# Kernel optimization log

Measured on AMD Instinct MI355X. Metric: run time of the kernel, lower is better.

The kernel has to match this reference:

```python
import jax, jax.numpy as jnp
import numpy as np

N, P, IN, HID, HEADS, OUT, E = 8192, 3, 256, 64, 8, 64, 262144
HD = HEADS * HID


def _gat(h, fc, al, ar, bias, src, dst):
    # DGL GATConv forward (no dropout), returns (elu(out) [N,H,D], attention [E,H])
    feat = (h @ fc).reshape(N, HEADS, HID)          # [N,H,D]
    el = (feat * al).sum(-1)                        # [N,H]
    er = (feat * ar).sum(-1)                        # [N,H]
    e = jax.nn.leaky_relu(el[src] + er[dst], negative_slope=0.2)  # [E,H]
    emax = jax.ops.segment_max(e, dst, num_segments=N)            # [N,H]
    ee = jnp.exp(e - emax[dst])
    denom = jax.ops.segment_sum(ee, dst, num_segments=N)          # [N,H]
    a = ee / denom[dst]                                           # edge softmax over dst
    rst = jax.ops.segment_sum(a[:, :, None] * feat[src], dst, num_segments=N)  # [N,H,D]
    out = jax.nn.elu(rst + bias)
    return out, a


def setup_inputs():
    key = jax.random.key(0)
    ks = jax.random.split(key, 12)
    s = 0.05
    return {
        "h": jax.random.normal(ks[0], (N, IN), jnp.float32),
        "edge_src": jax.random.randint(ks[1], (P, E), 0, N, jnp.int32),
        "edge_dst": jax.random.randint(ks[2], (P, E), 0, N, jnp.int32),
        "gat_fc": jax.random.normal(ks[3], (P, IN, HD), jnp.float32) * s,
        "attn_l": jax.random.normal(ks[4], (P, HEADS, HID), jnp.float32) * s,
        "attn_r": jax.random.normal(ks[5], (P, HEADS, HID), jnp.float32) * s,
        "gat_bias": jnp.zeros((P, HEADS, HID), jnp.float32),
        "sa_w1": jax.random.normal(ks[6], (HD, 128), jnp.float32) * s,
        "sa_b1": jnp.zeros((128,), jnp.float32),
        "sa_w2": jax.random.normal(ks[7], (128, 1), jnp.float32) * s,
        "pred_w": jax.random.normal(ks[8], (HD, OUT), jnp.float32) * s,
        "pred_b": jnp.zeros((OUT,), jnp.float32),
    }


def reference(h, edge_src, edge_dst, gat_fc, attn_l, attn_r, gat_bias,
              sa_w1, sa_b1, sa_w2, pred_w, pred_b):
    zp_list, alpha_list = [], []
    for p in range(P):
        z_p, a_p = _gat(h, gat_fc[p], attn_l[p], attn_r[p], gat_bias[p],
                        edge_src[p], edge_dst[p])
        zp_list.append(z_p.reshape(N, HD))          # flatten(start_dim=1)
        alpha_list.append(a_p.mean(axis=1))         # [E], mean over heads
    zp = jnp.stack(zp_list, axis=1)                 # [N,P,HD]

    # Semantic attention
    w = (zp @ sa_w1 + sa_b1) @ sa_w2                # [N,P,1]
    w = jax.nn.leaky_relu(w, negative_slope=0.01).mean(axis=0)  # [P,1]
    beta = jax.nn.softmax(w, axis=0)                # [P,1]

    # Dense adjacency accumulation of edge attention weights
    atten = jnp.zeros((N, N), jnp.float32)
    for p in range(P):
        vals = alpha_list[p] * beta[p, 0]
        atten = atten.at[edge_src[p], edge_dst[p]].add(vals)

    z = (beta[None, :, :] * zp).sum(axis=1)         # [N,HD]
    out = z @ pred_w + pred_b                       # [N,OUT]
    return out, atten
```

## Files before the change

kernel.cpp:

```cpp
#include <hip/hip_runtime.h>
#include <math.h>

#define NN    8192
#define PP    3
#define INF_  256
#define HID_  64
#define HEADS 8
#define OUTF  64
#define NE    262144
#define HD    512
#define DEGCAP 128
#define NB    4
#define DOFF  (NB * NN)
#define POFF  (NB * NN + 1)

typedef __attribute__((ext_vector_type(8))) short short8;
typedef __attribute__((ext_vector_type(4))) float f32x4;

__device__ __forceinline__ unsigned short f2bf(float f) {
    unsigned u = __float_as_uint(f);
    unsigned r = u + 0x7fffu + ((u >> 16) & 1u);
    return (unsigned short)(r >> 16);
}
__device__ __forceinline__ float bf2f_lo(unsigned v) { return __uint_as_float(v << 16); }
__device__ __forceinline__ float bf2f_hi(unsigned v) { return __uint_as_float(v & 0xffff0000u); }

__device__ __forceinline__ void beta_reg(const float* __restrict__ wsum,
                                         float& rb0, float& rb1, float& rb2) {
    int lane = threadIdx.x & 63;
    float s0 = wsum[lane], s1 = wsum[64 + lane], s2 = wsum[128 + lane];
#pragma unroll
    for (int off = 32; off > 0; off >>= 1) {
        s0 += __shfl_down(s0, off);
        s1 += __shfl_down(s1, off);
        s2 += __shfl_down(s2, off);
    }
    float t0 = __shfl(s0, 0), t1 = __shfl(s1, 0), t2 = __shfl(s2, 0);
    float w0 = t0 / (float)NN, w1 = t1 / (float)NN, w2 = t2 / (float)NN;
    float m  = fmaxf(w0, fmaxf(w1, w2));
    float e0 = expf(w0 - m), e1 = expf(w1 - m), e2 = expf(w2 - m);
    float ss = e0 + e1 + e2;
    rb0 = e0 / ss; rb1 = e1 / ss; rb2 = e2 / ss;
}

__global__ __launch_bounds__(256) void cast_count(
        const float* __restrict__ h, const float* __restrict__ fc,
        const int* __restrict__ esrc, const int* __restrict__ edst,
        unsigned short* __restrict__ hb, unsigned short* __restrict__ fcT,
        int* __restrict__ counts ,
        float* __restrict__ atten) {
    int b = blockIdx.x, t = threadIdx.x;
    if (b < 2048) {
        int i = b * 256 + t;
        float4 v = *(const float4*)(h + (size_t)i * 4);
        ushort4 o = { f2bf(v.x), f2bf(v.y), f2bf(v.z), f2bf(v.w) };
        *(ushort4*)(hb + (size_t)i * 4) = o;
    } else if (b < 2048 + 1536) {
        int i = (b - 2048) * 256 + t;
        if (i < PP * INF_ * HD) {
            int p = i / (INF_ * HD);
            int rem = i - p * INF_ * HD;
            int k = rem / HD;
            int n = rem - k * HD;
            fcT[(size_t)p * HD * INF_ + (size_t)n * INF_ + k] = f2bf(fc[i]);
        }
    } else if (b < 2048 + 1536 + 768) {
        int i = (b - 3584) * 256 + t;
        int4 s4 = ((const int4*)esrc)[i];
        int4 d4 = ((const int4*)edst)[i];
        int p = i >> 16;
        int base = p * DOFF;
        atomicAdd(&counts[base + (d4.x << 2) + (s4.x >> 11)], 1);
        atomicAdd(&counts[base + (d4.y << 2) + (s4.y >> 11)], 1);
        atomicAdd(&counts[base + (d4.z << 2) + (s4.z >> 11)], 1);
        atomicAdd(&counts[base + (d4.w << 2) + (s4.w >> 11)], 1);
    } else {
        f32x4* a4 = (f32x4*)atten;
        int idx0 = (b - 4352) * 256 + t;
        f32x4 zero = {0.f, 0.f, 0.f, 0.f};
#pragma unroll 4
        for (int it = 0; it < 64; ++it)
            __builtin_nontemporal_store(zero, &a4[(size_t)it * 262144 + idx0]);
    }
}

__global__ __launch_bounds__(1024) void scan_vw(
        const int* __restrict__ counts, int* __restrict__ offsets,
        int* __restrict__ cursor, const float* __restrict__ w1,
        const float* __restrict__ b1, const float* __restrict__ w2,
        float* __restrict__ v ) {
    int t = threadIdx.x;
    if (blockIdx.x == 3) {
        if (t < HD) {
            float s = 0.f;
            for (int k = 0; k < 128; ++k) s += w1[t * 128 + k] * w2[k];
            v[t] = s;
        } else if (t == HD) {
            float c = 0.f;
            for (int k = 0; k < 128; ++k) c += b1[k] * w2[k];
            v[HD] = c;
        }
        return;
    }
    __shared__ int sh[1024];
    int seg = blockIdx.x;
    const int* cnt = counts + seg * DOFF;
    int* offs = offsets + seg * POFF;
    int* cur  = cursor + seg * DOFF;
    int loc[32];
    int s = 0;
#pragma unroll
    for (int i = 0; i < 32; ++i) { loc[i] = cnt[t * 32 + i]; s += loc[i]; }
    sh[t] = s;
    __syncthreads();
    for (int off = 1; off < 1024; off <<= 1) {
        int vv = (t >= off) ? sh[t - off] : 0;
        __syncthreads();
        sh[t] += vv;
        __syncthreads();
    }
    int run = sh[t] - s;
#pragma unroll
    for (int i = 0; i < 32; ++i) {
        offs[t * 32 + i] = run;
        cur[t * 32 + i]  = run;
        run += loc[i];
    }
    if (t == 1023) offs[DOFF] = run;
}

#define LDK 72
__global__ __launch_bounds__(256) void scatter_gemm(
        const int* __restrict__ esrc, const int* __restrict__ edst,
        int* __restrict__ cursor, int* __restrict__ ssrc_sorted,
        const unsigned short* __restrict__ hb,
        const unsigned short* __restrict__ fcT,
        const float* __restrict__ al_all,
        const float* __restrict__ ar_all,
        unsigned short* __restrict__ featb,
        float* __restrict__ el,
        float* __restrict__ er) {
    __shared__ unsigned short As[64 * LDK];
    __shared__ unsigned short Bs[64 * LDK];
    int tid = threadIdx.x;
    if (blockIdx.x < 3072) {
        int i = blockIdx.x * 256 + tid;
        int p = i >> 18;
        int s = esrc[i], d = edst[i];
        int pos = atomicAdd(&cursor[p * DOFF + (d << 2) + (s >> 11)], 1);
        ssrc_sorted[(size_t)p * NE + pos] = s;
        return;
    }
    int g  = blockIdx.x - 3072;
    int p  = g >> 10;
    int n0 = (g & 7) * 64;
    int m0 = ((g >> 3) & 127) * 64;
    const unsigned short* Bt = fcT + (size_t)p * HD * INF_;
    unsigned short* C = featb + (size_t)p * NN * HD;
    int wv   = tid >> 6, lane = tid & 63;
    int row  = tid >> 2, kc = (tid & 3) * 8;
    int l16  = lane & 15, quad = lane >> 4;
    int mw   = wv * 16;
    f32x4 acc[4] = {{0.f,0.f,0.f,0.f},{0.f,0.f,0.f,0.f},
                    {0.f,0.f,0.f,0.f},{0.f,0.f,0.f,0.f}};
    for (int k0 = 0; k0 < INF_; k0 += 64) {
        const unsigned short* ha = &hb[(size_t)(m0 + row) * INF_ + k0 + kc];
        const unsigned short* ba = &Bt[(size_t)(n0 + row) * INF_ + k0 + kc];
        *(short8*)&As[row * LDK + kc]      = *(const short8*)ha;
        *(short8*)&As[row * LDK + kc + 32] = *(const short8*)(ha + 32);
        *(short8*)&Bs[row * LDK + kc]      = *(const short8*)ba;
        *(short8*)&Bs[row * LDK + kc + 32] = *(const short8*)(ba + 32);
        __syncthreads();
        short8 af0 = *(short8*)&As[(mw + l16) * LDK + quad * 8];
        short8 af1 = *(short8*)&As[(mw + l16) * LDK + 32 + quad * 8];
#pragma unroll
        for (int nt = 0; nt < 4; ++nt) {
            short8 bf0 = *(short8*)&Bs[(nt * 16 + l16) * LDK + quad * 8];
            acc[nt] = __builtin_amdgcn_mfma_f32_16x16x32_bf16(af0, bf0, acc[nt], 0, 0, 0);
            short8 bf1 = *(short8*)&Bs[(nt * 16 + l16) * LDK + 32 + quad * 8];
            acc[nt] = __builtin_amdgcn_mfma_f32_16x16x32_bf16(af1, bf1, acc[nt], 0, 0, 0);
        }
        __syncthreads();
    }
#pragma unroll
    for (int nt = 0; nt < 4; ++nt) {
#pragma unroll
        for (int r = 0; r < 4; ++r) {
            C[(size_t)(m0 + mw + quad * 4 + r) * HD + n0 + nt * 16 + l16] =
                f2bf(acc[nt][r]);
        }
    }
    int hidx = n0 >> 6;
    float alv[4], arv[4];
#pragma unroll
    for (int nt = 0; nt < 4; ++nt) {
        alv[nt] = al_all[p * HD + n0 + nt * 16 + l16];
        arv[nt] = ar_all[p * HD + n0 + nt * 16 + l16];
    }
    float* elp = el + (size_t)p * NN * HEADS;
    float* erp = er + (size_t)p * NN * HEADS;
#pragma unroll
    for (int r = 0; r < 4; ++r) {
        float pe = acc[0][r] * alv[0] + acc[1][r] * alv[1] +
                   acc[2][r] * alv[2] + acc[3][r] * alv[3];
        float pr = acc[0][r] * arv[0] + acc[1][r] * arv[1] +
                   acc[2][r] * arv[2] + acc[3][r] * arv[3];
#pragma unroll
        for (int m = 1; m < 16; m <<= 1) {
            pe += __shfl_xor(pe, m);
            pr += __shfl_xor(pr, m);
        }
        if (l16 == 0) {
            int node = m0 + mw + quad * 4 + r;
            elp[node * HEADS + hidx] = pe;
            erp[node * HEADS + hidx] = pr;
        }
    }
}

__global__ __launch_bounds__(256) void fused_attn_rst(
        const int* __restrict__ ssrc_sorted, const int* __restrict__ offsets_all,
        const float* __restrict__ el, const float* __restrict__ er,
        const unsigned short* __restrict__ featb,
        const float* __restrict__ bias_all, const float* __restrict__ v,
        float* __restrict__ alpha_all ,
        unsigned short* __restrict__ zpb,
        float* __restrict__ wsum ) {
    __shared__ float sh_e[4][DEGCAP * 8];
    __shared__ int   sh_src[4][DEGCAP];
    int wv = threadIdx.x >> 6, lane = threadIdx.x & 63;
    int gid = blockIdx.x * 4 + wv;
    int n = gid & (NN - 1);
    int p = gid >> 13;
    const int* srcrow  = ssrc_sorted + (size_t)p * NE;
    const int* offs    = offsets_all + p * POFF;
    const float* elp   = el + (size_t)p * NN * HEADS;
    const float* erp   = er + (size_t)p * NN * HEADS;
    const unsigned short* feat = featb + (size_t)p * NN * HD;
    int start = offs[n * NB];
    int deg = offs[n * NB + NB] - start;
    if (deg > DEGCAP) deg = DEGCAP;

    float4 r0 = *(const float4*)(erp + n * 8);
    float4 r1 = *(const float4*)(erp + n * 8 + 4);
    for (int t = lane; t < deg; t += 64) {
        int s = srcrow[start + t];
        sh_src[wv][t] = s;
        float4 l0 = *(const float4*)(elp + s * 8);
        float4 l1 = *(const float4*)(elp + s * 8 + 4);
        float sc[8] = {l0.x + r0.x, l0.y + r0.y, l0.z + r0.z, l0.w + r0.w,
                       l1.x + r1.x, l1.y + r1.y, l1.z + r1.z, l1.w + r1.w};
#pragma unroll
        for (int hh = 0; hh < 8; ++hh) {
            float x = sc[hh];
            sh_e[wv][t * 8 + hh] = x > 0.f ? x : 0.2f * x;
        }
    }
    __syncthreads();

    int h = lane >> 3;
    {
        int j = lane & 7;
        float m = -INFINITY;
        for (int t = j; t < deg; t += 8) m = fmaxf(m, sh_e[wv][t * 8 + h]);
#pragma unroll
        for (int off = 4; off; off >>= 1) m = fmaxf(m, __shfl_xor(m, off));
        float ssum = 0.f;
        for (int t = j; t < deg; t += 8) {
            float ee = __expf(sh_e[wv][t * 8 + h] - m);
            sh_e[wv][t * 8 + h] = ee;
            ssum += ee;
        }
#pragma unroll
        for (int off = 4; off; off >>= 1) ssum += __shfl_xor(ssum, off);
        float inv = 1.f / ssum;
        for (int t = j; t < deg; t += 8) sh_e[wv][t * 8 + h] *= inv;
    }
    __syncthreads();

    for (int t = lane; t < deg; t += 64) {
        float s = 0.f;
#pragma unroll
        for (int hh = 0; hh < 8; ++hh) s += sh_e[wv][t * 8 + hh];
        alpha_all[(size_t)p * NE + start + t] = s * 0.125f;
    }

    int c = lane * 8;
    float acc[8] = {0.f, 0.f, 0.f, 0.f, 0.f, 0.f, 0.f, 0.f};
#define FMA8(F, KI) { \
        float a_ = sh_e[wv][(KI) * 8 + h]; \
        acc[0] += a_ * bf2f_lo((F).x); acc[1] += a_ * bf2f_hi((F).x); \
        acc[2] += a_ * bf2f_lo((F).y); acc[3] += a_ * bf2f_hi((F).y); \
        acc[4] += a_ * bf2f_lo((F).z); acc[5] += a_ * bf2f_hi((F).z); \
        acc[6] += a_ * bf2f_lo((F).w); acc[7] += a_ * bf2f_hi((F).w); }
    int k = 0;
    for (; k + 4 <= deg; k += 4) {
        int s0 = sh_src[wv][k],     s1 = sh_src[wv][k + 1];
        int s2 = sh_src[wv][k + 2], s3 = sh_src[wv][k + 3];
        uint4 f0 = *(const uint4*)&feat[(size_t)s0 * HD + c];
        uint4 f1 = *(const uint4*)&feat[(size_t)s1 * HD + c];
        uint4 f2 = *(const uint4*)&feat[(size_t)s2 * HD + c];
        uint4 f3 = *(const uint4*)&feat[(size_t)s3 * HD + c];
        FMA8(f0, k); FMA8(f1, k + 1); FMA8(f2, k + 2); FMA8(f3, k + 3);
    }
    for (; k < deg; ++k) {
        int s = sh_src[wv][k];
        uint4 f = *(const uint4*)&feat[(size_t)s * HD + c];
        FMA8(f, k);
    }
#undef FMA8
    const float* bias = bias_all + p * HD;
    float4 b0 = *(const float4*)(bias + c);
    float4 b1 = *(const float4*)(bias + c + 4);
    float z[8];
    z[0] = acc[0] + b0.x; z[1] = acc[1] + b0.y; z[2] = acc[2] + b0.z; z[3] = acc[3] + b0.w;
    z[4] = acc[4] + b1.x; z[5] = acc[5] + b1.y; z[6] = acc[6] + b1.z; z[7] = acc[7] + b1.w;
#pragma unroll
    for (int i = 0; i < 8; ++i) z[i] = z[i] > 0.f ? z[i] : expm1f(z[i]);
    uint4 zo;
    zo.x = (unsigned)f2bf(z[0]) | ((unsigned)f2bf(z[1]) << 16);
    zo.y = (unsigned)f2bf(z[2]) | ((unsigned)f2bf(z[3]) << 16);
    zo.z = (unsigned)f2bf(z[4]) | ((unsigned)f2bf(z[5]) << 16);
    zo.w = (unsigned)f2bf(z[6]) | ((unsigned)f2bf(z[7]) << 16);
    *(uint4*)&zpb[(size_t)n * (PP * HD) + p * HD + c] = zo;

    float4 v0 = *(const float4*)(v + c);
    float4 v1 = *(const float4*)(v + c + 4);
    float part = z[0] * v0.x + z[1] * v0.y + z[2] * v0.z + z[3] * v0.w +
                 z[4] * v1.x + z[5] * v1.y + z[6] * v1.z + z[7] * v1.w;
#pragma unroll
    for (int off = 32; off > 0; off >>= 1) part += __shfl_down(part, off);
    if (lane == 0) {
        float w = part + v[HD];
        w = w > 0.f ? w : 0.01f * w;
        atomicAdd(&wsum[p * 64 + (n & 63)], w);
    }
}

#define K5R 16
__global__ __launch_bounds__(256) void final_atten(
        const unsigned short* __restrict__ zpb, const float* __restrict__ wsum,
        const float* __restrict__ pw, const float* __restrict__ pb,
        const int* __restrict__ ssrc_sorted, const int* __restrict__ offsets_all,
        const float* __restrict__ alpha,
        float* __restrict__ out, float* __restrict__ atten) {
    __shared__ float buf[NN];
    __shared__ int   sh_s[3 * DEGCAP];
    __shared__ int   sh_cnt;
    float b0, b1, b2;
    beta_reg(wsum, b0, b1, b2);
    int tid = threadIdx.x;
    if (blockIdx.x < NN) {
        int n = blockIdx.x;
        f32x4 zero = {0.f, 0.f, 0.f, 0.f};
        for (int j = tid; j < NN / 4; j += 256) ((f32x4*)buf)[j] = zero;
        if (tid == 0) sh_cnt = 0;
        __syncthreads();
        for (int p = 0; p < PP; ++p) {
            float bsel = p == 0 ? b0 : (p == 1 ? b1 : b2);
            const int* offs = offsets_all + p * POFF;
            int start = offs[n * NB];
            int deg = offs[n * NB + NB] - start;
            if (deg > DEGCAP) deg = DEGCAP;
            const int* srcrow = ssrc_sorted + (size_t)p * NE + start;
            const float* arow = alpha + (size_t)p * NE + start;
            for (int t = tid; t < deg; t += 256) {
                int s = srcrow[t];
                atomicAdd(&buf[s], arow[t] * bsel);
                int slot = atomicAdd(&sh_cnt, 1);
                sh_s[slot] = s;
            }
        }
        __syncthreads();
        int cnt = sh_cnt;
        for (int k = tid; k < cnt; k += 256) {
            int s = sh_s[k];
            __builtin_nontemporal_store(buf[s], &atten[(size_t)s * NN + n]);
        }
    } else {
        float* zt = buf;
        int n0 = (blockIdx.x - NN) * K5R;
        int c = tid * 2;
#pragma unroll
        for (int r = 0; r < K5R; ++r) {
            const unsigned short* zr = zpb + (size_t)(n0 + r) * (PP * HD);
            unsigned u0 = *(const unsigned*)(zr + c);
            unsigned u1 = *(const unsigned*)(zr + HD + c);
            unsigned u2 = *(const unsigned*)(zr + 2 * HD + c);
            zt[r * HD + c]     = b0 * bf2f_lo(u0) + b1 * bf2f_lo(u1) + b2 * bf2f_lo(u2);
            zt[r * HD + c + 1] = b0 * bf2f_hi(u0) + b1 * bf2f_hi(u1) + b2 * bf2f_hi(u2);
        }
        __syncthreads();
        int o = tid & 63, rg = tid >> 6;
        float a0 = 0.f, a1 = 0.f, a2 = 0.f, a3 = 0.f;
        for (int j = 0; j < HD; ++j) {
            float pwj = pw[j * 64 + o];
            a0 += zt[(rg * 4 + 0) * HD + j] * pwj;
            a1 += zt[(rg * 4 + 1) * HD + j] * pwj;
            a2 += zt[(rg * 4 + 2) * HD + j] * pwj;
            a3 += zt[(rg * 4 + 3) * HD + j] * pwj;
        }
        float bo = pb[o];
        out[(size_t)(n0 + rg * 4 + 0) * 64 + o] = a0 + bo;
        out[(size_t)(n0 + rg * 4 + 1) * 64 + o] = a1 + bo;
        out[(size_t)(n0 + rg * 4 + 2) * 64 + o] = a2 + bo;
        out[(size_t)(n0 + rg * 4 + 3) * 64 + o] = a3 + bo;
    }
}

extern "C" void kernel_launch(void* const* d_in, const int* in_sizes, int n_in,
                              void* d_out, int out_size, void* d_ws, size_t ws_size,
                              hipStream_t stream) {
    const float* h    = (const float*)d_in[0];
    const int*   esrc = (const int*)d_in[1];
    const int*   edst = (const int*)d_in[2];
    const float* fc   = (const float*)d_in[3];
    const float* al   = (const float*)d_in[4];
    const float* ar   = (const float*)d_in[5];
    const float* bias = (const float*)d_in[6];
    const float* w1   = (const float*)d_in[7];
    const float* b1   = (const float*)d_in[8];
    const float* w2   = (const float*)d_in[9];
    const float* pw   = (const float*)d_in[10];
    const float* pb   = (const float*)d_in[11];
    float* out   = (float*)d_out;
    float* atten = out + (size_t)NN * OUTF;

    char* ws = (char*)d_ws;
    size_t off = 0;
    auto alloc = [&](size_t bytes) {
        void* p = ws + off;
        off = (off + bytes + 255) & ~(size_t)255;
        return p;
    };
    unsigned short* zpb   = (unsigned short*)alloc(sizeof(short) * (size_t)NN * PP * HD);
    unsigned short* featb = (unsigned short*)alloc(sizeof(short) * (size_t)PP * NN * HD);
    unsigned short* hb  = (unsigned short*)alloc(sizeof(short) * (size_t)NN * INF_);
    unsigned short* fcT = (unsigned short*)alloc(sizeof(short) * (size_t)PP * HD * INF_);
    float*  el      = (float*)alloc(sizeof(float) * PP * NN * HEADS);
    float*  er      = (float*)alloc(sizeof(float) * PP * NN * HEADS);
    float*  alpha   = (float*)alloc(sizeof(float) * (size_t)PP * NE);
    int*    counts  = (int*)alloc(sizeof(int) * 3 * DOFF);
    float*  wsum    = (float*)alloc(sizeof(float) * 3 * 64);
    int*    offsets = (int*)alloc(sizeof(int) * 3 * POFF);
    int*    cursor  = (int*)alloc(sizeof(int) * 3 * DOFF);
    int*    ssrc_sorted = (int*)alloc(sizeof(int) * (size_t)PP * NE);
    float*  vbuf    = (float*)alloc(sizeof(float) * (HD + 1));

    (void)hipMemsetAsync(counts, 0, sizeof(int) * 3 * DOFF + 1024, stream);

    cast_count<<<2048 + 1536 + 768 + 1024, 256, 0, stream>>>(
        h, fc, esrc, edst, hb, fcT, counts, atten);

    scan_vw<<<4, 1024, 0, stream>>>(counts, offsets, cursor, w1, b1, w2, vbuf);

    scatter_gemm<<<6144, 256, 0, stream>>>(
        esrc, edst, cursor, ssrc_sorted,
        hb, fcT, al, ar, featb, el, er);

    fused_attn_rst<<<NN * PP / 4, 256, 0, stream>>>(
        ssrc_sorted, offsets, el, er, featb, bias, vbuf, alpha, zpb, wsum);

    final_atten<<<NN + NN / K5R, 256, 0, stream>>>(
        zpb, wsum, pw, pb, ssrc_sorted, offsets, alpha, out, atten);
}
```

Before: 604.2 us.

## Privatize edge counting and scatter into LDS per destination range

Edge-bucket counting and the bucketed scatter of source indices now use per-block shared-memory histograms and cursors, one block per (metapath, 512-destination range). This replaces the global atomics on the counts and cursor arrays, and removes the cursor buffer and its initialization in the scan. Each of the 48 blocks now streams the full edge list of its metapath and filters by destination range. That trades about 16x redundant edge reads and much lower block parallelism for LDS-speed atomics and fewer global atomic round trips.

```diff
diff --git a/kernel.cpp b/kernel.cpp
--- a/kernel.cpp
+++ b/kernel.cpp
@@ -11,6 +11,9 @@
 #define HD    512
 #define DEGCAP 128
 #define NB    4
+#define NRANGE 16
+#define RDST  (NN / NRANGE)
+#define RBINS (RDST * NB)
 #define DOFF  (NB * NN)
 #define POFF  (NB * NN + 1)
 
@@ -49,6 +52,7 @@
         unsigned short* __restrict__ hb, unsigned short* __restrict__ fcT,
         int* __restrict__ counts ,
         float* __restrict__ atten) {
+    __shared__ int hcnt[RBINS];
     int b = blockIdx.x, t = threadIdx.x;
     if (b < 2048) {
         int i = b * 256 + t;
@@ -64,29 +68,39 @@
             int n = rem - k * HD;
             fcT[(size_t)p * HD * INF_ + (size_t)n * INF_ + k] = f2bf(fc[i]);
         }
-    } else if (b < 2048 + 1536 + 768) {
-        int i = (b - 3584) * 256 + t;
-        int4 s4 = ((const int4*)esrc)[i];
-        int4 d4 = ((const int4*)edst)[i];
-        int p = i >> 16;
-        int base = p * DOFF;
-        atomicAdd(&counts[base + (d4.x << 2) + (s4.x >> 11)], 1);
-        atomicAdd(&counts[base + (d4.y << 2) + (s4.y >> 11)], 1);
-        atomicAdd(&counts[base + (d4.z << 2) + (s4.z >> 11)], 1);
-        atomicAdd(&counts[base + (d4.w << 2) + (s4.w >> 11)], 1);
-    } else {
+    } else if (b < 2048 + 1536 + 1024) {
         f32x4* a4 = (f32x4*)atten;
-        int idx0 = (b - 4352) * 256 + t;
+        int idx0 = (b - 3584) * 256 + t;
         f32x4 zero = {0.f, 0.f, 0.f, 0.f};
 #pragma unroll 4
         for (int it = 0; it < 64; ++it)
             __builtin_nontemporal_store(zero, &a4[(size_t)it * 262144 + idx0]);
+    } else {
+        int bb = b - 4608;
+        int p = bb >> 4, r = bb & 15;
+        int dbase = r << 9;
+        for (int j = t; j < RBINS; j += 256) hcnt[j] = 0;
+        __syncthreads();
+        const int4* s4p = (const int4*)esrc + p * 65536;
+        const int4* d4p = (const int4*)edst + p * 65536;
+        for (int g = t; g < 65536; g += 256) {
+            int4 s4 = s4p[g];
+            int4 d4 = d4p[g];
+            int d;
+            d = d4.x - dbase; if ((unsigned)d < (unsigned)RDST) atomicAdd(&hcnt[(d << 2) + (s4.x >> 11)], 1);
+            d = d4.y - dbase; if ((unsigned)d < (unsigned)RDST) atomicAdd(&hcnt[(d << 2) + (s4.y >> 11)], 1);
+            d = d4.z - dbase; if ((unsigned)d < (unsigned)RDST) atomicAdd(&hcnt[(d << 2) + (s4.z >> 11)], 1);
+            d = d4.w - dbase; if ((unsigned)d < (unsigned)RDST) atomicAdd(&hcnt[(d << 2) + (s4.w >> 11)], 1);
+        }
+        __syncthreads();
+        int* cbase = counts + p * DOFF + (dbase << 2);
+        for (int j = t; j < RBINS; j += 256) cbase[j] = hcnt[j];
     }
 }
 
 __global__ __launch_bounds__(1024) void scan_vw(
         const int* __restrict__ counts, int* __restrict__ offsets,
-        int* __restrict__ cursor, const float* __restrict__ w1,
+        const float* __restrict__ w1,
         const float* __restrict__ b1, const float* __restrict__ w2,
         float* __restrict__ v ) {
     int t = threadIdx.x;
@@ -106,7 +120,6 @@
     int seg = blockIdx.x;
     const int* cnt = counts + seg * DOFF;
     int* offs = offsets + seg * POFF;
-    int* cur  = cursor + seg * DOFF;
     int loc[32];
     int s = 0;
 #pragma unroll
@@ -123,7 +136,6 @@
 #pragma unroll
     for (int i = 0; i < 32; ++i) {
         offs[t * 32 + i] = run;
-        cur[t * 32 + i]  = run;
         run += loc[i];
     }
     if (t == 1023) offs[DOFF] = run;
@@ -132,7 +144,7 @@
 #define LDK 72
 __global__ __launch_bounds__(256) void scatter_gemm(
         const int* __restrict__ esrc, const int* __restrict__ edst,
-        int* __restrict__ cursor, int* __restrict__ ssrc_sorted,
+        const int* __restrict__ offsets_all, int* __restrict__ ssrc_sorted,
         const unsigned short* __restrict__ hb,
         const unsigned short* __restrict__ fcT,
         const float* __restrict__ al_all,
@@ -143,15 +155,28 @@
     __shared__ unsigned short As[64 * LDK];
     __shared__ unsigned short Bs[64 * LDK];
     int tid = threadIdx.x;
-    if (blockIdx.x < 3072) {
-        int i = blockIdx.x * 256 + tid;
-        int p = i >> 18;
-        int s = esrc[i], d = edst[i];
-        int pos = atomicAdd(&cursor[p * DOFF + (d << 2) + (s >> 11)], 1);
-        ssrc_sorted[(size_t)p * NE + pos] = s;
+    if (blockIdx.x < PP * NRANGE) {
+        int* cur = (int*)As;
+        int p = blockIdx.x >> 4, r = blockIdx.x & 15;
+        int dbase = r << 9;
+        const int* obase = offsets_all + p * POFF + (dbase << 2);
+        for (int j = tid; j < RBINS; j += 256) cur[j] = obase[j];
+        __syncthreads();
+        const int4* s4p = (const int4*)esrc + p * 65536;
+        const int4* d4p = (const int4*)edst + p * 65536;
+        int* outp = ssrc_sorted + (size_t)p * NE;
+        for (int g = tid; g < 65536; g += 256) {
+            int4 s4 = s4p[g];
+            int4 d4 = d4p[g];
+            int d, pos;
+            d = d4.x - dbase; if ((unsigned)d < (unsigned)RDST) { pos = atomicAdd(&cur[(d << 2) + (s4.x >> 11)], 1); outp[pos] = s4.x; }
+            d = d4.y - dbase; if ((unsigned)d < (unsigned)RDST) { pos = atomicAdd(&cur[(d << 2) + (s4.y >> 11)], 1); outp[pos] = s4.y; }
+            d = d4.z - dbase; if ((unsigned)d < (unsigned)RDST) { pos = atomicAdd(&cur[(d << 2) + (s4.z >> 11)], 1); outp[pos] = s4.z; }
+            d = d4.w - dbase; if ((unsigned)d < (unsigned)RDST) { pos = atomicAdd(&cur[(d << 2) + (s4.w >> 11)], 1); outp[pos] = s4.w; }
+        }
         return;
     }
-    int g  = blockIdx.x - 3072;
+    int g  = blockIdx.x - PP * NRANGE;
     int p  = g >> 10;
     int n0 = (g & 7) * 64;
     int m0 = ((g >> 3) & 127) * 64;
@@ -443,19 +468,18 @@
     int*    counts  = (int*)alloc(sizeof(int) * 3 * DOFF);
     float*  wsum    = (float*)alloc(sizeof(float) * 3 * 64);
     int*    offsets = (int*)alloc(sizeof(int) * 3 * POFF);
-    int*    cursor  = (int*)alloc(sizeof(int) * 3 * DOFF);
     int*    ssrc_sorted = (int*)alloc(sizeof(int) * (size_t)PP * NE);
     float*  vbuf    = (float*)alloc(sizeof(float) * (HD + 1));
 
-    (void)hipMemsetAsync(counts, 0, sizeof(int) * 3 * DOFF + 1024, stream);
-
-    cast_count<<<2048 + 1536 + 768 + 1024, 256, 0, stream>>>(
+    (void)hipMemsetAsync(wsum, 0, 1024, stream);
+
+    cast_count<<<2048 + 1536 + 1024 + PP * NRANGE, 256, 0, stream>>>(
         h, fc, esrc, edst, hb, fcT, counts, atten);
 
-    scan_vw<<<4, 1024, 0, stream>>>(counts, offsets, cursor, w1, b1, w2, vbuf);
-
-    scatter_gemm<<<6144, 256, 0, stream>>>(
-        esrc, edst, cursor, ssrc_sorted,
+    scan_vw<<<4, 1024, 0, stream>>>(counts, offsets, w1, b1, w2, vbuf);
+
+    scatter_gemm<<<PP * NRANGE + 3072, 256, 0, stream>>>(
+        esrc, edst, offsets, ssrc_sorted,
         hb, fcT, al, ar, featb, el, er);
 
     fused_attn_rst<<<NN * PP / 4, 256, 0, stream>>>(
```

Result: slower. 906.2 us (+50.0%).
